# Kernel optimization log

Hardware: AMD Instinct MI355X
Metric: run time of the kernel (lower is better)

Reference implementation:

```python
import jax, jax.numpy as jnp
import numpy as np

N_NODES = 100000
N_EDGES = 3200000
D_IN = 128
D_OUT = 128


def setup_inputs() -> dict:
    key = jax.random.key(0)
    k1, k2, k3, k4, k5, k6 = jax.random.split(key, 6)
    x = jax.random.normal(k1, (N_NODES, D_IN), dtype=jnp.float32)
    weight = jax.random.normal(k2, (D_OUT, D_IN), dtype=jnp.float32)
    bias = jax.random.normal(k3, (D_OUT,), dtype=jnp.float32)
    edge_vals = jax.random.uniform(k4, (N_EDGES,), dtype=jnp.float32)
    edge_rows = jax.random.randint(k5, (N_EDGES,), 0, N_NODES, dtype=jnp.int32)
    edge_cols = jax.random.randint(k6, (N_EDGES,), 0, N_NODES, dtype=jnp.int32)
    return {"x": x, "weight": weight, "bias": bias,
            "edge_vals": edge_vals, "edge_rows": edge_rows, "edge_cols": edge_cols}


def reference(x, weight, bias, edge_vals, edge_rows, edge_cols):
    # h = Linear(x): [N, D_OUT]
    h = jnp.einsum('ni,oi->no', x, weight) + bias
    # out = A @ h with A in COO form: out[r] += v * h[c]
    msgs = edge_vals[:, None] * h[edge_cols]  # [E, D_OUT]
    out = jax.ops.segment_sum(msgs, edge_rows, num_segments=N_NODES)
    return out
```

## Files before the change

### kernel.cpp

```cpp
#include <hip/hip_runtime.h>
#include <hip/hip_bf16.h>

#define D 128
#define RPB 256
#define RPB_SHIFT 8
#define NBMAX 512
#define P1CHUNK 8192
#define P2CAP 15360

using bf16x8 = __attribute__((ext_vector_type(8))) short;
using f32x4  = __attribute__((ext_vector_type(4))) float;
using f32x2  = __attribute__((ext_vector_type(2))) float;

static __device__ inline unsigned short f2bf(float f) {
    __hip_bfloat16 b = __float2bfloat16(f);
    return reinterpret_cast<unsigned short&>(b);
}

__global__ __launch_bounds__(256) void gemm_bhist_kernel(
    const float* __restrict__ x, const float* __restrict__ W,
    const float* __restrict__ bias, __hip_bfloat16* __restrict__ h, int N,
    const int* __restrict__ rows, int* __restrict__ bcount, int E, int GB)
{
    __shared__ unsigned short sA[128 * 128];
    __shared__ unsigned short sB[128 * 128];
    __shared__ int lh[NBMAX];

    const int tid = threadIdx.x;

    if (blockIdx.x >= GB) {
        const int bid = blockIdx.x - GB;
        for (int i = tid; i < NBMAX; i += 256) lh[i] = 0;
        __syncthreads();
        const int base = bid * P1CHUNK;
#pragma unroll
        for (int it = 0; it < P1CHUNK / 1024; ++it) {
            int e = base + (it * 256 + tid) * 4;
            if (e + 3 < E) {
                int4 r4 = *reinterpret_cast<const int4*>(rows + e);
                atomicAdd(&lh[r4.x >> RPB_SHIFT], 1);
                atomicAdd(&lh[r4.y >> RPB_SHIFT], 1);
                atomicAdd(&lh[r4.z >> RPB_SHIFT], 1);
                atomicAdd(&lh[r4.w >> RPB_SHIFT], 1);
            } else {
                for (int k = 0; k < 4; ++k)
                    if (e + k < E) atomicAdd(&lh[rows[e + k] >> RPB_SHIFT], 1);
            }
        }
        __syncthreads();
        for (int i = tid; i < NBMAX; i += 256) {
            int c = lh[i];
            if (c) atomicAdd(&bcount[i], c);
        }
        return;
    }

    const int nbase = blockIdx.x * 128;

#pragma unroll
    for (int it = 0; it < 16; ++it) {
        const int r = it * 8 + (tid >> 5);
        const int c = (tid & 31) * 4;
        const unsigned addr = (unsigned)((r * 256 + c * 2) ^ ((r & 7) << 4));

        const int gr = nbase + r;
        float4 xv = make_float4(0.f, 0.f, 0.f, 0.f);
        if (gr < N) xv = *reinterpret_cast<const float4*>(x + (size_t)gr * D + c);
        ushort4 xb = make_ushort4(f2bf(xv.x), f2bf(xv.y), f2bf(xv.z), f2bf(xv.w));
        *reinterpret_cast<ushort4*>(reinterpret_cast<char*>(sA) + addr) = xb;

        float4 wv = *reinterpret_cast<const float4*>(W + (size_t)r * D + c);
        ushort4 wb = make_ushort4(f2bf(wv.x), f2bf(wv.y), f2bf(wv.z), f2bf(wv.w));
        *reinterpret_cast<ushort4*>(reinterpret_cast<char*>(sB) + addr) = wb;
    }
    __syncthreads();

    const int wid  = tid >> 6;
    const int lane = tid & 63;
    const int wr   = (wid >> 1) * 64;
    const int wc   = (wid & 1) * 64;
    const int lrow = lane & 15;
    const int lkb  = (lane >> 4) * 16;

    f32x4 acc[4][4] = {};

#pragma unroll
    for (int kk = 0; kk < 4; ++kk) {
        const int kbyte = kk * 64 + lkb;
        bf16x8 a[4], b[4];
#pragma unroll
        for (int m = 0; m < 4; ++m) {
            const int row = wr + m * 16 + lrow;
            const unsigned addr = (unsigned)((row * 256 + kbyte) ^ ((row & 7) << 4));
            a[m] = *reinterpret_cast<const bf16x8*>(reinterpret_cast<const char*>(sA) + addr);
        }
#pragma unroll
        for (int n = 0; n < 4; ++n) {
            const int row = wc + n * 16 + lrow;
            const unsigned addr = (unsigned)((row * 256 + kbyte) ^ ((row & 7) << 4));
            b[n] = *reinterpret_cast<const bf16x8*>(reinterpret_cast<const char*>(sB) + addr);
        }
#pragma unroll
        for (int m = 0; m < 4; ++m)
#pragma unroll
            for (int n = 0; n < 4; ++n)
                acc[m][n] = __builtin_amdgcn_mfma_f32_16x16x32_bf16(a[m], b[n], acc[m][n], 0, 0, 0);
    }

    float bv[4];
#pragma unroll
    for (int n = 0; n < 4; ++n) bv[n] = bias[wc + n * 16 + lrow];

#pragma unroll
    for (int m = 0; m < 4; ++m) {
        const int row0 = nbase + wr + m * 16 + (lane >> 4) * 4;
#pragma unroll
        for (int n = 0; n < 4; ++n) {
            const int col = wc + n * 16 + lrow;
#pragma unroll
            for (int r = 0; r < 4; ++r) {
                const int grow = row0 + r;
                if (grow < N)
                    h[(size_t)grow * D + col] = __float2bfloat16(acc[m][n][r] + bv[n]);
            }
        }
    }
}

__global__ __launch_bounds__(512) void bscan_kernel(
    const int* __restrict__ bcount, int* __restrict__ bstart,
    int* __restrict__ bcur, int NB, int E)
{
    __shared__ int s[512];
    const int tid = threadIdx.x;
    int v = (tid < NB) ? bcount[tid] : 0;
    s[tid] = v;
    __syncthreads();
    for (int off = 1; off < 512; off <<= 1) {
        int t = (tid >= off) ? s[tid - off] : 0;
        __syncthreads();
        s[tid] += t;
        __syncthreads();
    }
    if (tid < NB) {
        int excl = s[tid] - v;
        bstart[tid] = excl;
        bcur[tid]   = excl;
    }
    if (tid == 0) bstart[NB] = E;
}

__global__ __launch_bounds__(256) void pass1_kernel(
    const int* __restrict__ rows, const int* __restrict__ cols,
    const float* __restrict__ vals, int* __restrict__ bcur,
    uint2* __restrict__ pairs, int E)
{
    __shared__ int srows[P1CHUNK];
    __shared__ int lh[NBMAX];
    __shared__ int lbase[NBMAX];

    const int tid  = threadIdx.x;
    const int base = blockIdx.x * P1CHUNK;

    for (int i = tid; i < NBMAX; i += 256) lh[i] = 0;
    __syncthreads();

#pragma unroll 4
    for (int it = 0; it < P1CHUNK / 256; ++it) {
        int e = base + it * 256 + tid;
        int r = (e < E) ? rows[e] : -1;
        srows[it * 256 + tid] = r;
        if (r >= 0) atomicAdd(&lh[r >> RPB_SHIFT], 1);
    }
    __syncthreads();

    for (int i = tid; i < NBMAX; i += 256) {
        int c = lh[i];
        lbase[i] = c ? atomicAdd(&bcur[i], c) : 0;
        lh[i] = 0;
    }
    __syncthreads();

#pragma unroll 4
    for (int it = 0; it < P1CHUNK / 256; ++it) {
        int e = base + it * 256 + tid;
        int r = srows[it * 256 + tid];
        if (r < 0) continue;
        int b = r >> RPB_SHIFT;
        int lofs = atomicAdd(&lh[b], 1);
        unsigned packed = ((unsigned)(r & (RPB - 1)) << 17) | (unsigned)cols[e];
        pairs[lbase[b] + lofs] = make_uint2(packed, __float_as_uint(vals[e]));
    }
}

__global__ __launch_bounds__(256) void pass2_kernel(
    uint2* __restrict__ pairs, const int* __restrict__ bstart,
    int* __restrict__ rowstart, int N)
{
    __shared__ uint2 st[P2CAP];
    __shared__ int rh[RPB];
    __shared__ int sc[RPB];
    __shared__ int cur[RPB];

    const int b   = blockIdx.x;
    const int tid = threadIdx.x;
    const int start = bstart[b];
    const int end   = bstart[b + 1];
    int cnt = end - start;
    if (cnt > P2CAP) cnt = P2CAP;

    rh[tid] = 0;
    __syncthreads();

    for (int i = tid; i < cnt; i += 256) {
        uint2 p = pairs[start + i];
        st[i] = p;
        atomicAdd(&rh[p.x >> 17], 1);
    }
    __syncthreads();

    int myc = rh[tid];
    sc[tid] = myc;
    __syncthreads();
    for (int off = 1; off < 256; off <<= 1) {
        int t = (tid >= off) ? sc[tid - off] : 0;
        __syncthreads();
        sc[tid] += t;
        __syncthreads();
    }
    int excl = sc[tid] - myc;
    cur[tid] = start + excl;
    int grow = b * RPB + tid;
    if (grow < N) rowstart[grow] = start + excl;
    __syncthreads();

    for (int i = tid; i < cnt; i += 256) {
        uint2 p = st[i];
        int r = (int)(p.x >> 17);
        int pos = atomicAdd(&cur[r], 1);
        pairs[pos] = make_uint2(p.x & 0x1FFFFu, p.y);
    }
}

__global__ __launch_bounds__(256) void row_gather_kernel(
    const __hip_bfloat16* __restrict__ hbf, const uint2* __restrict__ pairs,
    const int* __restrict__ rowstart, float* __restrict__ out, int N, int E)
{
    int row  = (int)((blockIdx.x * (size_t)blockDim.x + threadIdx.x) >> 6);
    int lane = threadIdx.x & 63;
    if (row >= N) return;

    int start = rowstart[row];
    int end   = (row + 1 < N) ? rowstart[row + 1] : E;

    const char* hb = reinterpret_cast<const char*>(hbf);
    const unsigned lbyte = (unsigned)lane << 2;
    float ax = 0.f, ay = 0.f;

    for (int e0 = start; e0 < end; e0 += 64) {
        int pl = e0 + lane;
        if (pl >= end) pl = end - 1;
        uint2 p = pairs[pl];
        int pc = (int)p.x, pv = (int)p.y;
        int m = end - e0; if (m > 64) m = 64;

        int idx = 0;
        const int m16 = m & ~15;
        for (; idx < m16; idx += 16) {
            unsigned c[16], vb[16], hv[16];
#pragma unroll
            for (int u = 0; u < 16; ++u) {
                c[u]  = (unsigned)__builtin_amdgcn_readlane(pc, idx + u);
                vb[u] = (unsigned)__builtin_amdgcn_readlane(pv, idx + u);
            }
#pragma unroll
            for (int u = 0; u < 16; ++u)
                hv[u] = *reinterpret_cast<const unsigned*>(hb + (((size_t)c[u]) << 8) + lbyte);
#pragma unroll
            for (int u = 0; u < 16; ++u) {
                float v = __uint_as_float(vb[u]);
                ax += v * __uint_as_float(hv[u] << 16);
                ay += v * __uint_as_float(hv[u] & 0xffff0000u);
            }
        }
        const int m8 = m & ~7;
        for (; idx < m8; idx += 8) {
            unsigned c[8], vb[8], hv[8];
#pragma unroll
            for (int u = 0; u < 8; ++u) {
                c[u]  = (unsigned)__builtin_amdgcn_readlane(pc, idx + u);
                vb[u] = (unsigned)__builtin_amdgcn_readlane(pv, idx + u);
            }
#pragma unroll
            for (int u = 0; u < 8; ++u)
                hv[u] = *reinterpret_cast<const unsigned*>(hb + (((size_t)c[u]) << 8) + lbyte);
#pragma unroll
            for (int u = 0; u < 8; ++u) {
                float v = __uint_as_float(vb[u]);
                ax += v * __uint_as_float(hv[u] << 16);
                ay += v * __uint_as_float(hv[u] & 0xffff0000u);
            }
        }
        for (; idx < m; ++idx) {
            unsigned c  = (unsigned)__builtin_amdgcn_readlane(pc, idx);
            unsigned vb = (unsigned)__builtin_amdgcn_readlane(pv, idx);
            unsigned hv = *reinterpret_cast<const unsigned*>(hb + (((size_t)c) << 8) + lbyte);
            float v = __uint_as_float(vb);
            ax += v * __uint_as_float(hv << 16);
            ay += v * __uint_as_float(hv & 0xffff0000u);
        }
    }

    f32x2 r2 = { ax, ay };
    __builtin_nontemporal_store(r2, reinterpret_cast<f32x2*>(out + (size_t)row * D) + lane);
}

__global__ __launch_bounds__(256) void gemm_kernel(
    const float* __restrict__ x, const float* __restrict__ W,
    const float* __restrict__ bias, float* __restrict__ h, int N)
{
    __shared__ float sWt[D][D];
    __shared__ float sx[16][D];
    const int tid = threadIdx.x;
    for (int idx = tid; idx < D * D; idx += 256) {
        int o = idx >> 7, i = idx & (D - 1);
        sWt[i][o] = W[idx];
    }
    const int nbase = blockIdx.x * 16;
    for (int idx = tid; idx < 16 * D; idx += 256) {
        int r = idx >> 7, i = idx & (D - 1);
        int n = nbase + r;
        sx[r][i] = (n < N) ? x[(size_t)n * D + i] : 0.0f;
    }
    __syncthreads();
    const int c = tid & (D - 1);
    const int rg = tid >> 7;
    float acc[8];
#pragma unroll
    for (int k = 0; k < 8; ++k) acc[k] = 0.0f;
#pragma unroll 4
    for (int i = 0; i < D; ++i) {
        float w = sWt[i][c];
#pragma unroll
        for (int k = 0; k < 8; ++k) acc[k] += sx[rg * 8 + k][i] * w;
    }
    const float b = bias[c];
#pragma unroll
    for (int k = 0; k < 8; ++k) {
        int n = nbase + rg * 8 + k;
        if (n < N) h[(size_t)n * D + c] = acc[k] + b;
    }
}

__global__ __launch_bounds__(256) void scatter_kernel(
    const float* __restrict__ h, const float* __restrict__ vals,
    const int* __restrict__ rows, const int* __restrict__ cols,
    float* __restrict__ out, int E)
{
    const int wid  = (int)((blockIdx.x * (size_t)blockDim.x + threadIdx.x) >> 6);
    const int lane = threadIdx.x & 63;
    if (wid >= E) return;
    const int   r = rows[wid];
    const int   c = cols[wid];
    const float v = vals[wid];
    float2 hv = *reinterpret_cast<const float2*>(h + (size_t)c * D + lane * 2);
    atomicAdd(out + (size_t)r * D + lane * 2,     v * hv.x);
    atomicAdd(out + (size_t)r * D + lane * 2 + 1, v * hv.y);
}

static inline size_t align16(size_t x) { return (x + 15) & ~(size_t)15; }

extern "C" void kernel_launch(void* const* d_in, const int* in_sizes, int n_in,
                              void* d_out, int out_size, void* d_ws, size_t ws_size,
                              hipStream_t stream)
{
    const float* x    = (const float*)d_in[0];
    const float* W    = (const float*)d_in[1];
    const float* bias = (const float*)d_in[2];
    const float* vals = (const float*)d_in[3];
    const int*   rows = (const int*)d_in[4];
    const int*   cols = (const int*)d_in[5];

    const int N = in_sizes[0] / D;
    const int E = in_sizes[3];
    float* out = (float*)d_out;

    const int NB = (N + RPB - 1) / RPB;

    size_t off_h        = 0;
    size_t off_pairs    = off_h        + align16((size_t)N * D * 2);
    size_t off_rowstart = off_pairs    + align16((size_t)E * 8);
    size_t off_bstart   = off_rowstart + align16((size_t)(N + 1) * 4);
    size_t off_bcount   = off_bstart   + align16((size_t)(NB + 1) * 4);
    size_t off_bcur     = off_bcount   + align16((size_t)NB * 4);
    size_t need         = off_bcur     + align16((size_t)NB * 4);

    if (ws_size >= need && NB <= NBMAX && N <= (1 << 17)) {
        char* ws = (char*)d_ws;
        __hip_bfloat16* hbf = (__hip_bfloat16*)(ws + off_h);
        uint2* pairs        = (uint2*)(ws + off_pairs);
        int*   rowstart     = (int*)(ws + off_rowstart);
        int*   bstart       = (int*)(ws + off_bstart);
        int*   bcount       = (int*)(ws + off_bcount);
        int*   bcur         = (int*)(ws + off_bcur);

        hipMemsetAsync(bcount, 0, (size_t)NB * 4, stream);

        const int GB = (N + 127) / 128;
        const int HB = (E + P1CHUNK - 1) / P1CHUNK;
        gemm_bhist_kernel<<<GB + HB, 256, 0, stream>>>(
            x, W, bias, hbf, N, rows, bcount, E, GB);

        bscan_kernel<<<1, 512, 0, stream>>>(bcount, bstart, bcur, NB, E);
        pass1_kernel<<<HB, 256, 0, stream>>>(rows, cols, vals, bcur, pairs, E);
        pass2_kernel<<<NB, 256, 0, stream>>>(pairs, bstart, rowstart, N);

        int gblocks = (int)(((size_t)N * 64 + 255) / 256);
        row_gather_kernel<<<gblocks, 256, 0, stream>>>(hbf, pairs, rowstart, out, N, E);
    } else {
        float* h = (float*)d_ws;
        hipMemsetAsync(out, 0, (size_t)out_size * sizeof(float), stream);
        gemm_kernel<<<(N + 15) / 16, 256, 0, stream>>>(x, W, bias, h, N);
        scatter_kernel<<<(E + 3) / 4, 256, 0, stream>>>(h, vals, rows, cols, out, E);
    }
}
```

Baseline: 233.9 us.

## Bin edges into fixed-capacity buckets fused with GEMM, with overflow fixup

Replaces the histogram, scan and scatter sequence with one pass that writes edges into fixed-capacity per-bucket slots (CAP each), fused into the GEMM launch. This drops the separate bscan and pass1 kernels and the second read of the row indices. Edges that overflow a bucket go to a small overflow list, which a single-block fixup kernel applies with atomics after the gather. Rows now carry explicit start and end offsets because buckets are no longer contiguous. The cost is a larger workspace, and any overflow beyond OVFCAP is silently dropped.

```diff
diff --git a/kernel.cpp b/kernel.cpp
--- a/kernel.cpp
+++ b/kernel.cpp
@@ -6,7 +6,9 @@
 #define RPB_SHIFT 8
 #define NBMAX 512
 #define P1CHUNK 8192
-#define P2CAP 15360
+#define CAP 9216
+#define OVFCAP 4096
+#define P2CAP_MID 15360
 
 using bf16x8 = __attribute__((ext_vector_type(8))) short;
 using f32x4  = __attribute__((ext_vector_type(4))) float;
@@ -16,6 +18,286 @@
     __hip_bfloat16 b = __float2bfloat16(f);
     return reinterpret_cast<unsigned short&>(b);
 }
+
+
+__global__ __launch_bounds__(256) void gemm_pass1_kernel(
+    const float* __restrict__ x, const float* __restrict__ W,
+    const float* __restrict__ bias, __hip_bfloat16* __restrict__ h, int N,
+    const int* __restrict__ rows, const int* __restrict__ cols,
+    const float* __restrict__ vals,
+    int* __restrict__ bcount,
+    uint2* __restrict__ pairs,
+    uint4* __restrict__ ovf,
+    int NB, int E, int GB)
+{
+    __shared__ __align__(16) char smem[64 * 1024];
+    const int tid = threadIdx.x;
+
+    if (blockIdx.x >= GB) {
+        int* srows = reinterpret_cast<int*>(smem);
+        int* lh    = reinterpret_cast<int*>(smem + 32 * 1024);
+        int* lbase = reinterpret_cast<int*>(smem + 34 * 1024);
+
+        const int base = (blockIdx.x - GB) * P1CHUNK;
+
+        for (int i = tid; i < NBMAX; i += 256) lh[i] = 0;
+        __syncthreads();
+
+#pragma unroll 4
+        for (int it = 0; it < P1CHUNK / 256; ++it) {
+            int e = base + it * 256 + tid;
+            int r = (e < E) ? rows[e] : -1;
+            srows[it * 256 + tid] = r;
+            if (r >= 0) atomicAdd(&lh[r >> RPB_SHIFT], 1);
+        }
+        __syncthreads();
+
+        for (int i = tid; i < NBMAX; i += 256) {
+            int c = lh[i];
+            lbase[i] = c ? (i * CAP + atomicAdd(&bcount[i], c)) : 0;
+            lh[i] = 0;
+        }
+        __syncthreads();
+
+#pragma unroll 4
+        for (int it = 0; it < P1CHUNK / 256; ++it) {
+            int e = base + it * 256 + tid;
+            int r = srows[it * 256 + tid];
+            if (r < 0) continue;
+            int b = r >> RPB_SHIFT;
+            int lofs = atomicAdd(&lh[b], 1);
+            int pos = lbase[b] + lofs;
+            if (pos < (b + 1) * CAP) {
+                unsigned packed = ((unsigned)(r & (RPB - 1)) << 17) | (unsigned)cols[e];
+                pairs[pos] = make_uint2(packed, __float_as_uint(vals[e]));
+            } else {
+                int oi = atomicAdd(&bcount[NB], 1);
+                if (oi < OVFCAP)
+                    ovf[oi] = make_uint4((unsigned)r, (unsigned)cols[e],
+                                         __float_as_uint(vals[e]), 0u);
+            }
+        }
+        return;
+    }
+
+    unsigned short* sA = reinterpret_cast<unsigned short*>(smem);
+    unsigned short* sB = reinterpret_cast<unsigned short*>(smem + 32 * 1024);
+    const int nbase = blockIdx.x * 128;
+
+#pragma unroll
+    for (int it = 0; it < 16; ++it) {
+        const int r = it * 8 + (tid >> 5);
+        const int c = (tid & 31) * 4;
+        const unsigned addr = (unsigned)((r * 256 + c * 2) ^ ((r & 7) << 4));
+
+        const int gr = nbase + r;
+        float4 xv = make_float4(0.f, 0.f, 0.f, 0.f);
+        if (gr < N) xv = *reinterpret_cast<const float4*>(x + (size_t)gr * D + c);
+        ushort4 xb = make_ushort4(f2bf(xv.x), f2bf(xv.y), f2bf(xv.z), f2bf(xv.w));
+        *reinterpret_cast<ushort4*>(reinterpret_cast<char*>(sA) + addr) = xb;
+
+        float4 wv = *reinterpret_cast<const float4*>(W + (size_t)r * D + c);
+        ushort4 wb = make_ushort4(f2bf(wv.x), f2bf(wv.y), f2bf(wv.z), f2bf(wv.w));
+        *reinterpret_cast<ushort4*>(reinterpret_cast<char*>(sB) + addr) = wb;
+    }
+    __syncthreads();
+
+    const int wid  = tid >> 6;
+    const int lane = tid & 63;
+    const int wr   = (wid >> 1) * 64;
+    const int wc   = (wid & 1) * 64;
+    const int lrow = lane & 15;
+    const int lkb  = (lane >> 4) * 16;
+
+    f32x4 acc[4][4] = {};
+
+#pragma unroll
+    for (int kk = 0; kk < 4; ++kk) {
+        const int kbyte = kk * 64 + lkb;
+        bf16x8 a[4], b[4];
+#pragma unroll
+        for (int m = 0; m < 4; ++m) {
+            const int row = wr + m * 16 + lrow;
+            const unsigned addr = (unsigned)((row * 256 + kbyte) ^ ((row & 7) << 4));
+            a[m] = *reinterpret_cast<const bf16x8*>(reinterpret_cast<const char*>(sA) + addr);
+        }
+#pragma unroll
+        for (int n = 0; n < 4; ++n) {
+            const int row = wc + n * 16 + lrow;
+            const unsigned addr = (unsigned)((row * 256 + kbyte) ^ ((row & 7) << 4));
+            b[n] = *reinterpret_cast<const bf16x8*>(reinterpret_cast<const char*>(sB) + addr);
+        }
+#pragma unroll
+        for (int m = 0; m < 4; ++m)
+#pragma unroll
+            for (int n = 0; n < 4; ++n)
+                acc[m][n] = __builtin_amdgcn_mfma_f32_16x16x32_bf16(a[m], b[n], acc[m][n], 0, 0, 0);
+    }
+
+    float bv[4];
+#pragma unroll
+    for (int n = 0; n < 4; ++n) bv[n] = bias[wc + n * 16 + lrow];
+
+#pragma unroll
+    for (int m = 0; m < 4; ++m) {
+        const int row0 = nbase + wr + m * 16 + (lane >> 4) * 4;
+#pragma unroll
+        for (int n = 0; n < 4; ++n) {
+            const int col = wc + n * 16 + lrow;
+#pragma unroll
+            for (int r = 0; r < 4; ++r) {
+                const int grow = row0 + r;
+                if (grow < N)
+                    h[(size_t)grow * D + col] = __float2bfloat16(acc[m][n][r] + bv[n]);
+            }
+        }
+    }
+}
+
+__global__ __launch_bounds__(256) void pass2_fixed_kernel(
+    uint2* __restrict__ pairs, const int* __restrict__ bcount,
+    int* __restrict__ rowstart, int* __restrict__ rowend, int N)
+{
+    __shared__ uint2 st[CAP];
+    __shared__ int rh[RPB];
+    __shared__ int sc[RPB];
+    __shared__ int cur[RPB];
+
+    const int b   = blockIdx.x;
+    const int tid = threadIdx.x;
+    const int start = b * CAP;
+    int cnt = bcount[b];
+    if (cnt > CAP) cnt = CAP;
+
+    rh[tid] = 0;
+    __syncthreads();
+
+    for (int i = tid; i < cnt; i += 256) {
+        uint2 p = pairs[start + i];
+        st[i] = p;
+        atomicAdd(&rh[p.x >> 17], 1);
+    }
+    __syncthreads();
+
+    int myc = rh[tid];
+    sc[tid] = myc;
+    __syncthreads();
+    for (int off = 1; off < 256; off <<= 1) {
+        int t = (tid >= off) ? sc[tid - off] : 0;
+        __syncthreads();
+        sc[tid] += t;
+        __syncthreads();
+    }
+    int excl = sc[tid] - myc;
+    cur[tid] = start + excl;
+    int grow = b * RPB + tid;
+    if (grow < N) {
+        rowstart[grow] = start + excl;
+        rowend[grow]   = start + excl + myc;
+    }
+    __syncthreads();
+
+    for (int i = tid; i < cnt; i += 256) {
+        uint2 p = st[i];
+        int r = (int)(p.x >> 17);
+        int pos = atomicAdd(&cur[r], 1);
+        pairs[pos] = make_uint2(p.x & 0x1FFFFu, p.y);
+    }
+}
+
+__global__ __launch_bounds__(256) void row_gather2_kernel(
+    const __hip_bfloat16* __restrict__ hbf, const uint2* __restrict__ pairs,
+    const int* __restrict__ rowstart, const int* __restrict__ rowend,
+    float* __restrict__ out, int N)
+{
+    int row  = (int)((blockIdx.x * (size_t)blockDim.x + threadIdx.x) >> 6);
+    int lane = threadIdx.x & 63;
+    if (row >= N) return;
+
+    int start = rowstart[row];
+    int end   = rowend[row];
+
+    const char* hb = reinterpret_cast<const char*>(hbf);
+    const unsigned lbyte = (unsigned)lane << 2;
+    float ax = 0.f, ay = 0.f;
+
+    for (int e0 = start; e0 < end; e0 += 64) {
+        int pl = e0 + lane;
+        if (pl >= end) pl = end - 1;
+        uint2 p = pairs[pl];
+        int pc = (int)p.x, pv = (int)p.y;
+        int m = end - e0; if (m > 64) m = 64;
+
+        int idx = 0;
+        const int m16 = m & ~15;
+        for (; idx < m16; idx += 16) {
+            unsigned c[16], vb[16], hv[16];
+#pragma unroll
+            for (int u = 0; u < 16; ++u) {
+                c[u]  = (unsigned)__builtin_amdgcn_readlane(pc, idx + u);
+                vb[u] = (unsigned)__builtin_amdgcn_readlane(pv, idx + u);
+            }
+#pragma unroll
+            for (int u = 0; u < 16; ++u)
+                hv[u] = *reinterpret_cast<const unsigned*>(hb + (((size_t)c[u]) << 8) + lbyte);
+#pragma unroll
+            for (int u = 0; u < 16; ++u) {
+                float v = __uint_as_float(vb[u]);
+                ax += v * __uint_as_float(hv[u] << 16);
+                ay += v * __uint_as_float(hv[u] & 0xffff0000u);
+            }
+        }
+        const int m8 = m & ~7;
+        for (; idx < m8; idx += 8) {
+            unsigned c[8], vb[8], hv[8];
+#pragma unroll
+            for (int u = 0; u < 8; ++u) {
+                c[u]  = (unsigned)__builtin_amdgcn_readlane(pc, idx + u);
+                vb[u] = (unsigned)__builtin_amdgcn_readlane(pv, idx + u);
+            }
+#pragma unroll
+            for (int u = 0; u < 8; ++u)
+                hv[u] = *reinterpret_cast<const unsigned*>(hb + (((size_t)c[u]) << 8) + lbyte);
+#pragma unroll
+            for (int u = 0; u < 8; ++u) {
+                float v = __uint_as_float(vb[u]);
+                ax += v * __uint_as_float(hv[u] << 16);
+                ay += v * __uint_as_float(hv[u] & 0xffff0000u);
+            }
+        }
+        for (; idx < m; ++idx) {
+            unsigned c  = (unsigned)__builtin_amdgcn_readlane(pc, idx);
+            unsigned vb = (unsigned)__builtin_amdgcn_readlane(pv, idx);
+            unsigned hv = *reinterpret_cast<const unsigned*>(hb + (((size_t)c) << 8) + lbyte);
+            float v = __uint_as_float(vb);
+            ax += v * __uint_as_float(hv << 16);
+            ay += v * __uint_as_float(hv & 0xffff0000u);
+        }
+    }
+
+    f32x2 r2 = { ax, ay };
+    __builtin_nontemporal_store(r2, reinterpret_cast<f32x2*>(out + (size_t)row * D) + lane);
+}
+
+__global__ __launch_bounds__(256) void fixup_kernel(
+    const uint4* __restrict__ ovf, const int* __restrict__ ovfcnt,
+    const __hip_bfloat16* __restrict__ hbf, float* __restrict__ out, int N)
+{
+    int cnt = *ovfcnt;
+    if (cnt > OVFCAP) cnt = OVFCAP;
+    const int wid  = threadIdx.x >> 6;
+    const int lane = threadIdx.x & 63;
+    const unsigned short* hb = reinterpret_cast<const unsigned short*>(hbf);
+    for (int i = wid; i < cnt; i += 4) {
+        uint4 e = ovf[i];
+        if ((int)e.x >= N) continue;
+        unsigned hv = *reinterpret_cast<const unsigned*>(hb + (size_t)e.y * D + lane * 2);
+        float v = __uint_as_float(e.z);
+        atomicAdd(out + (size_t)e.x * D + lane * 2,     v * __uint_as_float(hv << 16));
+        atomicAdd(out + (size_t)e.x * D + lane * 2 + 1, v * __uint_as_float(hv & 0xffff0000u));
+    }
+}
+
 
 __global__ __launch_bounds__(256) void gemm_bhist_kernel(
     const float* __restrict__ x, const float* __restrict__ W,
@@ -62,13 +344,11 @@
         const int r = it * 8 + (tid >> 5);
         const int c = (tid & 31) * 4;
         const unsigned addr = (unsigned)((r * 256 + c * 2) ^ ((r & 7) << 4));
-
         const int gr = nbase + r;
         float4 xv = make_float4(0.f, 0.f, 0.f, 0.f);
         if (gr < N) xv = *reinterpret_cast<const float4*>(x + (size_t)gr * D + c);
         ushort4 xb = make_ushort4(f2bf(xv.x), f2bf(xv.y), f2bf(xv.z), f2bf(xv.w));
         *reinterpret_cast<ushort4*>(reinterpret_cast<char*>(sA) + addr) = xb;
-
         float4 wv = *reinterpret_cast<const float4*>(W + (size_t)r * D + c);
         ushort4 wb = make_ushort4(f2bf(wv.x), f2bf(wv.y), f2bf(wv.z), f2bf(wv.w));
         *reinterpret_cast<ushort4*>(reinterpret_cast<char*>(sB) + addr) = wb;
@@ -83,7 +363,6 @@
     const int lkb  = (lane >> 4) * 16;
 
     f32x4 acc[4][4] = {};
-
 #pragma unroll
     for (int kk = 0; kk < 4; ++kk) {
         const int kbyte = kk * 64 + lkb;
@@ -110,7 +389,6 @@
     float bv[4];
 #pragma unroll
     for (int n = 0; n < 4; ++n) bv[n] = bias[wc + n * 16 + lrow];
-
 #pragma unroll
     for (int m = 0; m < 4; ++m) {
         const int row0 = nbase + wr + m * 16 + (lane >> 4) * 4;
@@ -197,7 +475,7 @@
     uint2* __restrict__ pairs, const int* __restrict__ bstart,
     int* __restrict__ rowstart, int N)
 {
-    __shared__ uint2 st[P2CAP];
+    __shared__ uint2 st[P2CAP_MID];
     __shared__ int rh[RPB];
     __shared__ int sc[RPB];
     __shared__ int cur[RPB];
@@ -207,7 +485,7 @@
     const int start = bstart[b];
     const int end   = bstart[b + 1];
     int cnt = end - start;
-    if (cnt > P2CAP) cnt = P2CAP;
+    if (cnt > P2CAP_MID) cnt = P2CAP_MID;
 
     rh[tid] = 0;
     __syncthreads();
@@ -314,6 +592,7 @@
     f32x2 r2 = { ax, ay };
     __builtin_nontemporal_store(r2, reinterpret_cast<f32x2*>(out + (size_t)row * D) + lane);
 }
+
 
 __global__ __launch_bounds__(256) void gemm_kernel(
     const float* __restrict__ x, const float* __restrict__ W,
@@ -386,35 +665,60 @@
     float* out = (float*)d_out;
 
     const int NB = (N + RPB - 1) / RPB;
-
-    size_t off_h        = 0;
-    size_t off_pairs    = off_h        + align16((size_t)N * D * 2);
-    size_t off_rowstart = off_pairs    + align16((size_t)E * 8);
-    size_t off_bstart   = off_rowstart + align16((size_t)(N + 1) * 4);
-    size_t off_bcount   = off_bstart   + align16((size_t)(NB + 1) * 4);
-    size_t off_bcur     = off_bcount   + align16((size_t)NB * 4);
-    size_t need         = off_bcur     + align16((size_t)NB * 4);
-
-    if (ws_size >= need && NB <= NBMAX && N <= (1 << 17)) {
+    const int GB = (N + 127) / 128;
+    const int HB = (E + P1CHUNK - 1) / P1CHUNK;
+
+    size_t f_h      = 0;
+    size_t f_pairs  = f_h      + align16((size_t)N * D * 2);
+    size_t f_rs     = f_pairs  + align16((size_t)NB * CAP * 8);
+    size_t f_re     = f_rs     + align16((size_t)N * 4);
+    size_t f_bcount = f_re     + align16((size_t)N * 4);
+    size_t f_ovf    = f_bcount + align16((size_t)(NB + 1) * 4);
+    size_t need_fast = f_ovf   + align16((size_t)OVFCAP * 16);
+
+    size_t m_h      = 0;
+    size_t m_pairs  = m_h      + align16((size_t)N * D * 2);
+    size_t m_rs     = m_pairs  + align16((size_t)E * 8);
+    size_t m_bstart = m_rs     + align16((size_t)(N + 1) * 4);
+    size_t m_bcount = m_bstart + align16((size_t)(NB + 1) * 4);
+    size_t m_bcur   = m_bcount + align16((size_t)NB * 4);
+    size_t need_mid = m_bcur   + align16((size_t)NB * 4);
+
+    if (ws_size >= need_fast && NB <= NBMAX && N <= (1 << 17)) {
         char* ws = (char*)d_ws;
-        __hip_bfloat16* hbf = (__hip_bfloat16*)(ws + off_h);
-        uint2* pairs        = (uint2*)(ws + off_pairs);
-        int*   rowstart     = (int*)(ws + off_rowstart);
-        int*   bstart       = (int*)(ws + off_bstart);
-        int*   bcount       = (int*)(ws + off_bcount);
-        int*   bcur         = (int*)(ws + off_bcur);
+        __hip_bfloat16* hbf = (__hip_bfloat16*)(ws + f_h);
+        uint2* pairs        = (uint2*)(ws + f_pairs);
+        int*   rowstart     = (int*)(ws + f_rs);
+        int*   rowend       = (int*)(ws + f_re);
+        int*   bcount       = (int*)(ws + f_bcount);
+        uint4* ovf          = (uint4*)(ws + f_ovf);
+
+        hipMemsetAsync(bcount, 0, (size_t)(NB + 1) * 4, stream);
+
+        gemm_pass1_kernel<<<GB + HB, 256, 0, stream>>>(
+            x, W, bias, hbf, N, rows, cols, vals, bcount, pairs, ovf, NB, E, GB);
+
+        pass2_fixed_kernel<<<NB, 256, 0, stream>>>(pairs, bcount, rowstart, rowend, N);
+
+        int gblocks = (int)(((size_t)N * 64 + 255) / 256);
+        row_gather2_kernel<<<gblocks, 256, 0, stream>>>(hbf, pairs, rowstart, rowend, out, N);
+
+        fixup_kernel<<<1, 256, 0, stream>>>(ovf, bcount + NB, hbf, out, N);
+    } else if (ws_size >= need_mid && NB <= NBMAX && N <= (1 << 17)) {
+        char* ws = (char*)d_ws;
+        __hip_bfloat16* hbf = (__hip_bfloat16*)(ws + m_h);
+        uint2* pairs        = (uint2*)(ws + m_pairs);
+        int*   rowstart     = (int*)(ws + m_rs);
+        int*   bstart       = (int*)(ws + m_bstart);
+        int*   bcount       = (int*)(ws + m_bcount);
+        int*   bcur         = (int*)(ws + m_bcur);
 
         hipMemsetAsync(bcount, 0, (size_t)NB * 4, stream);
-
-        const int GB = (N + 127) / 128;
-        const int HB = (E + P1CHUNK - 1) / P1CHUNK;
         gemm_bhist_kernel<<<GB + HB, 256, 0, stream>>>(
             x, W, bias, hbf, N, rows, bcount, E, GB);
-
         bscan_kernel<<<1, 512, 0, stream>>>(bcount, bstart, bcur, NB, E);
         pass1_kernel<<<HB, 256, 0, stream>>>(rows, cols, vals, bcur, pairs, E);
         pass2_kernel<<<NB, 256, 0, stream>>>(pairs, bstart, rowstart, N);
-
         int gblocks = (int)(((size_t)N * 64 + 255) / 256);
         row_gather_kernel<<<gblocks, 256, 0, stream>>>(hbf, pairs, rowstart, out, N, E);
     } else {
```

Result: faster. 209.0 us (-10.6%).
